# Performance work log

Measured on AMD Instinct MI355X. Metric: run time of the kernel, lower is better.

## Reference

```python
import jax, jax.numpy as jnp
import numpy as np

N, E, H = 20000, 320000, 5
IND, OUT = 64, 64
D2 = 2 * OUT          # 128
CAT = OUT + D2        # 192
BN_EPS = 1e-5


def _bn(x, g, b, m, v):
    # eval-mode BatchNorm1d
    return (x - m) * jax.lax.rsqrt(v + BN_EPS) * g + b


def _gcn(x, W, b, src, dst, n):
    # PyG GCNConv: add self-loops (already in src/dst), sym-normalized aggregation
    h = x @ W                                             # [N, C]
    deg = jax.ops.segment_sum(jnp.ones_like(dst, dtype=h.dtype), dst, num_segments=n)
    dinv = jnp.where(deg > 0, jax.lax.rsqrt(deg), 0.0)
    norm = dinv[src] * dinv[dst]                          # [E']
    out = jax.ops.segment_sum(h[src] * norm[:, None], dst, num_segments=n)
    return out + b


def _gat(x, W, att_src, att_dst, b, src, dst, n, heads, c):
    # PyG GATConv (concat=False): per-edge attention, segment softmax over dst
    hx = (x @ W).reshape(n, heads, c)                     # [N, H, C]
    a_s = jnp.einsum('nhc,hc->nh', hx, att_src)           # [N, H]
    a_d = jnp.einsum('nhc,hc->nh', hx, att_dst)
    e = jax.nn.leaky_relu(a_s[src] + a_d[dst], 0.2)       # [E', H]
    m = jax.ops.segment_max(e, dst, num_segments=n)       # every node has a self-loop
    w = jnp.exp(e - m[dst])
    den = jax.ops.segment_sum(w, dst, num_segments=n)
    alpha = w / den[dst]                                  # [E', H]
    out = jax.ops.segment_sum(hx[src] * alpha[:, :, None], dst, num_segments=n)  # [N,H,C]
    return out.mean(axis=1) + b


def setup_inputs() -> dict:
    key = jax.random.key(0)
    ks = iter(jax.random.split(key, 64))
    rn = lambda *s: jax.random.normal(next(ks), s, dtype=jnp.float32) * 0.05
    d = {}
    d['x_in'] = jax.random.normal(next(ks), (N, IND), dtype=jnp.float32)
    d['edge_index'] = jax.random.randint(next(ks), (2, E), 0, N, dtype=jnp.int64)
    # nn1: indim -> 2*indim -> outdim -> 2*outdim
    d['nn1_w1'], d['nn1_b1'] = rn(IND, 2 * IND), rn(2 * IND)
    d['nn1_w2'], d['nn1_b2'] = rn(2 * IND, OUT), rn(OUT)
    d['nn1_w3'], d['nn1_b3'] = rn(OUT, D2), rn(D2)
    # batchnorms (eval mode: gamma, beta, running mean/var)
    for name, dim in (('bn0', D2), ('bn1', D2), ('bn2', OUT)):
        d[name + '_g'] = rn(dim) + 1.0
        d[name + '_b'] = rn(dim)
        d[name + '_m'] = rn(dim)
        d[name + '_v'] = jax.random.uniform(next(ks), (dim,), jnp.float32, 0.5, 1.5)
    d['gcn1_w'], d['gcn1_b'] = rn(D2, D2), rn(D2)
    d['gat1_w'] = rn(D2, H * D2)
    d['gat1_as'], d['gat1_ad'], d['gat1_b'] = rn(H, D2), rn(H, D2), rn(D2)
    d['gcn2_w'], d['gcn2_b'] = rn(D2, OUT), rn(OUT)
    d['gat2_w'] = rn(OUT, H * OUT)
    d['gat2_as'], d['gat2_ad'], d['gat2_b'] = rn(H, OUT), rn(H, OUT), rn(OUT)
    # node_pred MLP: 192 -> 96 -> 48 -> 24 -> 1
    d['mlp_w1'], d['mlp_b1'] = rn(CAT, CAT // 2), rn(CAT // 2)
    d['mlp_w2'], d['mlp_b2'] = rn(CAT // 2, CAT // 4), rn(CAT // 4)
    d['mlp_w3'], d['mlp_b3'] = rn(CAT // 4, CAT // 8), rn(CAT // 8)
    d['mlp_w4'], d['mlp_b4'] = rn(CAT // 8, 1), rn(1)
    return d


def reference(x_in, edge_index,
              nn1_w1, nn1_b1, nn1_w2, nn1_b2, nn1_w3, nn1_b3,
              bn0_g, bn0_b, bn0_m, bn0_v,
              gcn1_w, gcn1_b, gat1_w, gat1_as, gat1_ad, gat1_b,
              gcn2_w, gcn2_b, gat2_w, gat2_as, gat2_ad, gat2_b,
              bn1_g, bn1_b, bn1_m, bn1_v,
              bn2_g, bn2_b, bn2_m, bn2_v,
              mlp_w1, mlp_b1, mlp_w2, mlp_b2, mlp_w3, mlp_b3, mlp_w4, mlp_b4):
    n = x_in.shape[0]
    loop = jnp.arange(n, dtype=edge_index.dtype)
    src = jnp.concatenate([edge_index[0], loop])   # self-loops (GCN & GAT defaults)
    dst = jnp.concatenate([edge_index[1], loop])

    sp = jax.nn.softplus
    x = sp(x_in @ nn1_w1 + nn1_b1)
    x = sp(x @ nn1_w2 + nn1_b2)
    x = x @ nn1_w3 + nn1_b3
    x = jax.nn.leaky_relu(_bn(x, bn0_g, bn0_b, bn0_m, bn0_v), 0.01)

    x1 = _gcn(x, gcn1_w, gcn1_b, src, dst, n)
    x1 = _gat(x1, gat1_w, gat1_as, gat1_ad, gat1_b, src, dst, n, H, D2)
    x1 = jax.nn.leaky_relu(_bn(x1, bn1_g, bn1_b, bn1_m, bn1_v), 0.01)
    skip1 = x + x1

    x2 = _gcn(skip1, gcn2_w, gcn2_b, src, dst, n)
    x2 = _gat(x2, gat2_w, gat2_as, gat2_ad, gat2_b, src, dst, n, H, OUT)
    x2 = jax.nn.leaky_relu(_bn(x2, bn2_g, bn2_b, bn2_m, bn2_v), 0.01)

    xf = jnp.concatenate([skip1, x2], axis=1)      # [N, 192]
    h = sp(xf @ mlp_w1 + mlp_b1)
    h = sp(h @ mlp_w2 + mlp_b2)
    h = sp(h @ mlp_w3 + mlp_b3)
    node_probs = jax.nn.sigmoid(h @ mlp_w4 + mlp_b4)   # [N, 1]
    return xf, node_probs
```

## Files before the change

kernel.cpp:

```cpp
#include <hip/hip_runtime.h>
#include <hip/hip_bf16.h>
#include <math.h>
#include <stdint.h>

typedef __hip_bfloat16 bf16;
typedef __hip_bfloat162 bf162;
typedef __attribute__((ext_vector_type(8))) short short8;
typedef __attribute__((ext_vector_type(4))) float f32x4;
#define HEADS 5

static inline long long cdivll(long long a, long long b){ return (a + b - 1) / b; }

__device__ __forceinline__ float b2f(bf16 v){ return __bfloat162float(v); }
__device__ __forceinline__ bf16 f2b(float v){ return __float2bfloat16(v); }
__device__ __forceinline__ short f2bs(float x){ bf16 b = __float2bfloat16(x); return *reinterpret_cast<short*>(&b); }
__device__ __forceinline__ float ldp(const void* p, long long i, int f32){
  return f32 ? ((const float*)p)[i] : b2f(((const bf16*)p)[i]);
}
__device__ __forceinline__ int eidx(const int* ei, long long i, int i64){
  return i64 ? ei[2 * i] : ei[i];
}
__device__ __forceinline__ float lrelu(float x, float a){ return x >= 0.f ? x : a * x; }
__device__ __forceinline__ float splus(float x){ return fmaxf(x, 0.f) + log1pf(expf(-fabsf(x))); }

__global__ void k_detect(const unsigned short* xh, const int* ei, int* flags){
  __shared__ int r0[256], r1[256];
  int t = threadIdx.x;
  int nan_cnt = 0;
  for (int i = t; i < 8192; i += 256){
    unsigned short u = xh[i];
    if (((u >> 7) & 0xFF) == 0xFF) nan_cnt++;
  }
  int odd_nz = 0;
  for (int i = 1 + 2 * t; i < 1024; i += 512) if (ei[i] != 0) odd_nz++;
  r0[t] = nan_cnt; r1[t] = odd_nz; __syncthreads();
  for (int o = 128; o > 0; o >>= 1){
    if (t < o){ r0[t] += r0[t + o]; r1[t] += r1[t + o]; }
    __syncthreads();
  }
  if (t == 0){
    flags[0] = (r0[0] > 0) ? 1 : 0;
    flags[1] = (r1[0] == 0) ? 1 : 0;
  }
}

__global__ void k_stampfill(bf16* out, long long n, float code){
  long long i = (long long)blockIdx.x * blockDim.x + threadIdx.x;
  if (i < n) out[i] = f2b(i == 0 ? code : 0.f);
}

__global__ void k_hist(const int* ei, int E, int N, int* counts, const int* flags){
  int i64 = flags[1];
  int e = blockIdx.x * blockDim.x + threadIdx.x;
  if (e >= E + N) return;
  int d = (e < E) ? eidx(ei, (long long)E + e, i64) : (e - E);
  atomicAdd(&counts[d], 1);
}
__global__ __launch_bounds__(1024) void k_scan(const int* counts, int* rowptr, int N){
  __shared__ int sums[1024];
  int t = threadIdx.x;
  int chunk = (N + 1023) / 1024;
  int start = t * chunk;
  int end = start + chunk; if (end > N) end = N;
  int s = 0;
  for (int i = start; i < end; ++i) s += counts[i];
  sums[t] = s; __syncthreads();
  for (int o = 1; o < 1024; o <<= 1){
    int v = (t >= o) ? sums[t - o] : 0;
    __syncthreads();
    sums[t] += v;
    __syncthreads();
  }
  int run = (t == 0) ? 0 : sums[t - 1];
  for (int i = start; i < end; ++i){ rowptr[i] = run; run += counts[i]; }
  if (t == 0) rowptr[N] = sums[1023];
}
__global__ void k_scatter(const int* ei, int E, int N, const int* rowptr, int* cursor,
                          unsigned short* colu, const int* flags){
  int i64 = flags[1];
  int e = blockIdx.x * blockDim.x + threadIdx.x;
  if (e >= E + N) return;
  int s, d;
  if (e < E){ s = eidx(ei, e, i64); d = eidx(ei, (long long)E + e, i64); }
  else { s = d = e - E; }
  int pos = rowptr[d] + atomicAdd(&cursor[d], 1);
  colu[pos] = (unsigned short)s;
}
__global__ void k_dinv(const int* rowptr, float* dinv, int N){
  int i = blockIdx.x * blockDim.x + threadIdx.x;
  if (i < N) dinv[i] = rsqrtf((float)(rowptr[i + 1] - rowptr[i]));
}

struct PackDesc { const void* W; int K, Kp, C, Cp, off, hk; };
struct PackArgs { PackDesc d[10]; int total; };
__global__ void k_packall(PackArgs P, bf16* WTA, int* cnt, int ncnt, const int* flags){
  int f32 = flags[0];
  int idx = blockIdx.x * blockDim.x + threadIdx.x;
  if (idx >= P.total){
    int z = idx - P.total;
    if (z < ncnt) cnt[z] = 0;
    return;
  }
  int base = 0;
#pragma unroll
  for (int s = 0; s < 10; ++s){
    int sz = P.d[s].Kp * P.d[s].Cp;
    if (idx < base + sz){
      int local = idx - base;
      int c = local / P.d[s].Kp;
      int k = local - c * P.d[s].Kp;
      float v;
      if (P.d[s].hk){
        int h = k / P.d[s].K;
        int kk = k - h * P.d[s].K;
        v = (c < P.d[s].C)
          ? ldp(P.d[s].W, (long long)kk * (P.d[s].hk * P.d[s].C) + h * P.d[s].C + c, f32) : 0.f;
      } else {
        v = (k < P.d[s].K && c < P.d[s].C)
          ? ldp(P.d[s].W, (long long)k * P.d[s].C + c, f32) : 0.f;
      }
      WTA[P.d[s].off + local] = f2b(v);
      return;
    }
    base += sz;
  }
}

__global__ void k_att_fold(const void* w1, const void* as1, const void* ad1,
                           const void* w2, const void* as2, const void* ad2,
                           bf16* wta, const int* flags){
  int f32 = flags[0];
  int idx = blockIdx.x * blockDim.x + threadIdx.x;
  if (idx < 8192){
    int c = idx >> 7, k = idx & 127;
    float v = 0.f;
    if (c < 10){
      int h = (c < 5) ? c : c - 5;
      const void* aw = (c < 5) ? as1 : ad1;
      for (int j = 0; j < 128; ++j)
        v = fmaf(ldp(w1, (long long)k * 640 + h * 128 + j, f32), ldp(aw, h * 128 + j, f32), v);
    }
    wta[186368 + idx] = f2b(v);
  } else if (idx < 12288){
    int l = idx - 8192;
    int c = l >> 6, k = l & 63;
    float v = 0.f;
    if (c < 10){
      int h = (c < 5) ? c : c - 5;
      const void* aw = (c < 5) ? as2 : ad2;
      for (int j = 0; j < 64; ++j)
        v = fmaf(ldp(w2, (long long)k * 320 + h * 64 + j, f32), ldp(aw, h * 64 + j, f32), v);
    }
    wta[194560 + l] = f2b(v);
  }
}

__global__ __launch_bounds__(256) void k_proj128(
    const void* in, int ik, int ldin, const bf16* WT, bf16* outb,
    int N, int Cp, const int* flags)
{
  __shared__ float red[2][16][68];
  int f32 = flags[0];
  int use_b16 = (ik == 2 && !f32);
  int t = threadIdx.x;
  int wave = t >> 6, lane = t & 63;
  int quad = lane >> 4, l15 = lane & 15;
  int rowgrp = wave & 1, kh = wave >> 1;
  int mbase = blockIdx.x * 32 + rowgrp * 16;
  int c0 = blockIdx.y * 64;
  f32x4 acc[4];
#pragma unroll
  for (int j = 0; j < 4; ++j) acc[j] = (f32x4){0.f, 0.f, 0.f, 0.f};

  int m = mbase + l15; if (m > N - 1) m = N - 1;

#pragma unroll
  for (int ki = 0; ki < 2; ++ki){
    int ka = kh * 64 + ki * 32 + quad * 8;
    short8 af;
    if (use_b16){
      af = *(const short8*)((const bf16*)in + (size_t)m * ldin + ka);
    } else {
      const float* p = (const float*)in + (size_t)m * ldin + ka;
      float4 v0 = *(const float4*)p;
      float4 v1 = *(const float4*)(p + 4);
      af[0] = f2bs(v0.x); af[1] = f2bs(v0.y); af[2] = f2bs(v0.z); af[3] = f2bs(v0.w);
      af[4] = f2bs(v1.x); af[5] = f2bs(v1.y); af[6] = f2bs(v1.z); af[7] = f2bs(v1.w);
    }
#pragma unroll
    for (int j = 0; j < 4; ++j){
      short8 bvv = *(const short8*)(WT + (size_t)(c0 + 16 * j + l15) * 128 + ka);
      acc[j] = __builtin_amdgcn_mfma_f32_16x16x32_bf16(af, bvv, acc[j], 0, 0, 0);
    }
  }

  if (kh == 1){
#pragma unroll
    for (int j = 0; j < 4; ++j)
#pragma unroll
      for (int r = 0; r < 4; ++r)
        red[rowgrp][quad * 4 + r][16 * j + l15] = acc[j][r];
  }
  __syncthreads();
  if (kh == 1) return;
#pragma unroll
  for (int j = 0; j < 4; ++j)
#pragma unroll
    for (int r = 0; r < 4; ++r)
      acc[j][r] += red[rowgrp][quad * 4 + r][16 * j + l15];

#pragma unroll
  for (int j = 0; j < 4; ++j){
    int c = c0 + 16 * j + l15;
#pragma unroll
    for (int r = 0; r < 4; ++r){
      int n = mbase + quad * 4 + r;
      if (n < N) outb[(size_t)n * Cp + c] = f2b(acc[j][r]);
    }
  }
}

__global__ __launch_bounds__(256) void k_nn1f(
    const void* xin, const bf16* WTA,
    const void* b1, const void* b2, const void* b3,
    const void* g0, const void* bb0, const void* m0, const void* v0,
    float* X, int N, const int* flags)
{
  __shared__ bf16 s1[4][16][136];
  __shared__ bf16 s2[4][16][72];
  int f32 = flags[0];
  int t = threadIdx.x, wave = t >> 6, lane = t & 63;
  int quad = lane >> 4, l15 = lane & 15;
  int mbase = blockIdx.x * 64 + wave * 16;
  int m = mbase + l15; if (m > N - 1) m = N - 1;

  f32x4 a1[8];
#pragma unroll
  for (int j = 0; j < 8; ++j) a1[j] = (f32x4){0.f, 0.f, 0.f, 0.f};
#pragma unroll
  for (int k0 = 0; k0 < 64; k0 += 32){
    int ka = k0 + quad * 8;
    short8 af;
    if (!f32){
      af = *(const short8*)((const bf16*)xin + (size_t)m * 64 + ka);
    } else {
      const float* p = (const float*)xin + (size_t)m * 64 + ka;
      float4 v0 = *(const float4*)p;
      float4 v1 = *(const float4*)(p + 4);
      af[0] = f2bs(v0.x); af[1] = f2bs(v0.y); af[2] = f2bs(v0.z); af[3] = f2bs(v0.w);
      af[4] = f2bs(v1.x); af[5] = f2bs(v1.y); af[6] = f2bs(v1.z); af[7] = f2bs(v1.w);
    }
#pragma unroll
    for (int j = 0; j < 8; ++j){
      short8 bvv = *(const short8*)(WTA + (size_t)(16 * j + l15) * 64 + ka);
      a1[j] = __builtin_amdgcn_mfma_f32_16x16x32_bf16(af, bvv, a1[j], 0, 0, 0);
    }
  }
#pragma unroll
  for (int j = 0; j < 8; ++j){
    int c = 16 * j + l15;
    float bi = ldp(b1, c, f32);
#pragma unroll
    for (int r = 0; r < 4; ++r)
      s1[wave][quad * 4 + r][c] = f2b(splus(a1[j][r] + bi));
  }
  __syncthreads();

  f32x4 a2[4];
#pragma unroll
  for (int j = 0; j < 4; ++j) a2[j] = (f32x4){0.f, 0.f, 0.f, 0.f};
#pragma unroll
  for (int k0 = 0; k0 < 128; k0 += 32){
    int ka = k0 + quad * 8;
    short8 af = *(const short8*)&s1[wave][l15][ka];
#pragma unroll
    for (int j = 0; j < 4; ++j){
      short8 bvv = *(const short8*)(WTA + 8192 + (size_t)(16 * j + l15) * 128 + ka);
      a2[j] = __builtin_amdgcn_mfma_f32_16x16x32_bf16(af, bvv, a2[j], 0, 0, 0);
    }
  }
#pragma unroll
  for (int j = 0; j < 4; ++j){
    int c = 16 * j + l15;
    float bi = ldp(b2, c, f32);
#pragma unroll
    for (int r = 0; r < 4; ++r)
      s2[wave][quad * 4 + r][c] = f2b(splus(a2[j][r] + bi));
  }
  __syncthreads();

  f32x4 a3[8];
#pragma unroll
  for (int j = 0; j < 8; ++j) a3[j] = (f32x4){0.f, 0.f, 0.f, 0.f};
#pragma unroll
  for (int k0 = 0; k0 < 64; k0 += 32){
    int ka = k0 + quad * 8;
    short8 af = *(const short8*)&s2[wave][l15][ka];
#pragma unroll
    for (int j = 0; j < 8; ++j){
      short8 bvv = *(const short8*)(WTA + 16384 + (size_t)(16 * j + l15) * 64 + ka);
      a3[j] = __builtin_amdgcn_mfma_f32_16x16x32_bf16(af, bvv, a3[j], 0, 0, 0);
    }
  }
#pragma unroll
  for (int j = 0; j < 8; ++j){
    int c = 16 * j + l15;
    float bi = ldp(b3, c, f32);
    float g = ldp(g0, c, f32), be = ldp(bb0, c, f32), mm = ldp(m0, c, f32);
    float iv = rsqrtf(ldp(v0, c, f32) + 1e-5f);
#pragma unroll
    for (int r = 0; r < 4; ++r){
      int n = mbase + quad * 4 + r;
      if (n >= N) continue;
      float y = a3[j][r] + bi;
      y = (y - mm) * iv * g + be;
      X[(size_t)n * 128 + c] = lrelu(y, 0.01f);
    }
  }
}

__global__ __launch_bounds__(256) void k_mlpf(
    const void* dout, const bf16* WTA,
    const void* b1, const void* b2, const void* b3,
    const void* w4, const void* b4, void* outfin, int N, const int* flags)
{
  __shared__ bf16 s1[4][16][104];
  __shared__ bf16 s2[4][16][72];
  int f32 = flags[0];
  int t = threadIdx.x, wave = t >> 6, lane = t & 63;
  int quad = lane >> 4, l15 = lane & 15;
  int mbase = blockIdx.x * 64 + wave * 16;
  int m = mbase + l15; if (m > N - 1) m = N - 1;

  f32x4 a1[6];
#pragma unroll
  for (int j = 0; j < 6; ++j) a1[j] = (f32x4){0.f, 0.f, 0.f, 0.f};
#pragma unroll
  for (int k0 = 0; k0 < 192; k0 += 32){
    int ka = k0 + quad * 8;
    short8 af;
    if (!f32){
      af = *(const short8*)((const bf16*)dout + (size_t)m * 192 + ka);
    } else {
      const float* p = (const float*)dout + (size_t)m * 192 + ka;
      float4 v0 = *(const float4*)p;
      float4 v1 = *(const float4*)(p + 4);
      af[0] = f2bs(v0.x); af[1] = f2bs(v0.y); af[2] = f2bs(v0.z); af[3] = f2bs(v0.w);
      af[4] = f2bs(v1.x); af[5] = f2bs(v1.y); af[6] = f2bs(v1.z); af[7] = f2bs(v1.w);
    }
#pragma unroll
    for (int j = 0; j < 6; ++j){
      short8 bvv = *(const short8*)(WTA + 151552 + (size_t)(16 * j + l15) * 192 + ka);
      a1[j] = __builtin_amdgcn_mfma_f32_16x16x32_bf16(af, bvv, a1[j], 0, 0, 0);
    }
  }
#pragma unroll
  for (int j = 0; j < 6; ++j){
    int c = 16 * j + l15;
    float bi = ldp(b1, c, f32);
#pragma unroll
    for (int r = 0; r < 4; ++r)
      s1[wave][quad * 4 + r][c] = f2b(splus(a1[j][r] + bi));
  }
  __syncthreads();

  f32x4 a2[3];
#pragma unroll
  for (int j = 0; j < 3; ++j) a2[j] = (f32x4){0.f, 0.f, 0.f, 0.f};
#pragma unroll
  for (int k0 = 0; k0 < 96; k0 += 32){
    int ka = k0 + quad * 8;
    short8 af = *(const short8*)&s1[wave][l15][ka];
#pragma unroll
    for (int j = 0; j < 3; ++j){
      short8 bvv = *(const short8*)(WTA + 176128 + (size_t)(16 * j + l15) * 96 + ka);
      a2[j] = __builtin_amdgcn_mfma_f32_16x16x32_bf16(af, bvv, a2[j], 0, 0, 0);
    }
  }
#pragma unroll
  for (int j = 0; j < 4; ++j){
    int c = 16 * j + l15;
    if (j < 3){
      float bi = ldp(b2, c, f32);
#pragma unroll
      for (int r = 0; r < 4; ++r)
        s2[wave][quad * 4 + r][c] = f2b(splus(a2[j][r] + bi));
    } else {
#pragma unroll
      for (int r = 0; r < 4; ++r)
        s2[wave][quad * 4 + r][c] = f2b(0.f);
    }
  }
  __syncthreads();

  f32x4 a3[2];
#pragma unroll
  for (int j = 0; j < 2; ++j) a3[j] = (f32x4){0.f, 0.f, 0.f, 0.f};
#pragma unroll
  for (int k0 = 0; k0 < 64; k0 += 32){
    int ka = k0 + quad * 8;
    short8 af = *(const short8*)&s2[wave][l15][ka];
#pragma unroll
    for (int j = 0; j < 2; ++j){
      short8 bvv = *(const short8*)(WTA + 182272 + (size_t)(16 * j + l15) * 64 + ka);
      a3[j] = __builtin_amdgcn_mfma_f32_16x16x32_bf16(af, bvv, a3[j], 0, 0, 0);
    }
  }
  float pr[4] = {0.f, 0.f, 0.f, 0.f};
#pragma unroll
  for (int j = 0; j < 2; ++j){
    int c = 16 * j + l15;
    float w = (c < 24) ? ldp(w4, c, f32) : 0.f;
    float bi = (c < 24) ? ldp(b3, c, f32) : 0.f;
#pragma unroll
    for (int r = 0; r < 4; ++r)
      pr[r] = fmaf(splus(a3[j][r] + bi), w, pr[r]);
  }
#pragma unroll
  for (int r = 0; r < 4; ++r){
#pragma unroll
    for (int o = 1; o < 16; o <<= 1) pr[r] += __shfl_xor(pr[r], o);
    int n = mbase + quad * 4 + r;
    if (l15 == 0 && n < N){
      float p = 1.f / (1.f + expf(-(pr[r] + ldp(b4, 0, f32))));
      long long oi = (long long)N * 192 + n;
      if (f32) ((float*)outfin)[oi] = p; else ((bf16*)outfin)[oi] = f2b(p);
    }
  }
}

__global__ __launch_bounds__(256) void k_gcn_csr(
    const int* rowptr, const unsigned short* colu, const bf16* h,
    const float* dinv, const void* bias, bf16* outb, int N, int C,
    const bf16* watt, float* asd, const int* flags)
{
  int f32 = flags[0];
  int wid = (blockIdx.x * 256 + threadIdx.x) >> 6;
  int lane = threadIdx.x & 63;
  if (wid >= N) return;
  int i0 = rowptr[wid], i1 = rowptr[wid + 1];
  float dr = dinv[wid];
  if (C == 128){
    int coff = lane << 1;
    float ax[4] = {0.f, 0.f, 0.f, 0.f}, ay[4] = {0.f, 0.f, 0.f, 0.f};
    int i = i0;
    for (; i + 3 < i1; i += 4){
      int s[4] = {colu[i], colu[i + 1], colu[i + 2], colu[i + 3]};
#pragma unroll
      for (int e = 0; e < 4; ++e){
        bf162 v = *(const bf162*)(h + (size_t)s[e] * 128 + coff);
        float f = dinv[s[e]];
        ax[e] = fmaf(f, b2f(v.x), ax[e]); ay[e] = fmaf(f, b2f(v.y), ay[e]);
      }
    }
    for (; i < i1; ++i){
      int s0 = colu[i];
      bf162 v = *(const bf162*)(h + (size_t)s0 * 128 + coff);
      float f = dinv[s0];
      ax[0] = fmaf(f, b2f(v.x), ax[0]); ay[0] = fmaf(f, b2f(v.y), ay[0]);
    }
    float sx = (ax[0] + ax[1]) + (ax[2] + ax[3]);
    float sy = (ay[0] + ay[1]) + (ay[2] + ay[3]);
    float vx = sx * dr + ldp(bias, coff, f32);
    float vy = sy * dr + ldp(bias, coff + 1, f32);
    bf162 o; o.x = f2b(vx); o.y = f2b(vy);
    *(bf162*)(outb + (size_t)wid * 128 + coff) = o;
    if (watt){
      float myv = 0.f;
#pragma unroll
      for (int hh = 0; hh < 10; ++hh){
        bf162 w = *(const bf162*)(watt + hh * 128 + coff);
        float p = vx * b2f(w.x) + vy * b2f(w.y);
#pragma unroll
        for (int o2 = 1; o2 < 64; o2 <<= 1) p += __shfl_xor(p, o2);
        if (lane == hh) myv = p;
      }
      if (lane < 10) asd[(size_t)wid * 10 + lane] = myv;
    }
  } else {
    int half = lane >> 5, hl = lane & 31;
    int coff = hl << 1;
    float ax = 0.f, ay = 0.f, bx = 0.f, by = 0.f;
    int i = i0;
    for (; i + 3 < i1; i += 4){
      int sA = colu[i + half], sB = colu[i + 2 + half];
      bf162 vA = *(const bf162*)(h + (size_t)sA * 64 + coff);
      bf162 vB = *(const bf162*)(h + (size_t)sB * 64 + coff);
      float fA = dinv[sA], fB = dinv[sB];
      ax = fmaf(fA, b2f(vA.x), ax); ay = fmaf(fA, b2f(vA.y), ay);
      bx = fmaf(fB, b2f(vB.x), bx); by = fmaf(fB, b2f(vB.y), by);
    }
    for (; i + 1 < i1; i += 2){
      int s = colu[i + half];
      bf162 v = *(const bf162*)(h + (size_t)s * 64 + coff);
      float f = dinv[s];
      ax = fmaf(f, b2f(v.x), ax); ay = fmaf(f, b2f(v.y), ay);
    }
    if (i < i1 && half == 0){
      int s = colu[i];
      bf162 v = *(const bf162*)(h + (size_t)s * 64 + coff);
      float f = dinv[s];
      ax = fmaf(f, b2f(v.x), ax); ay = fmaf(f, b2f(v.y), ay);
    }
    ax += bx; ay += by;
    ax += __shfl_xor(ax, 32);
    ay += __shfl_xor(ay, 32);
    float vx = ax * dr + ldp(bias, coff, f32);
    float vy = ay * dr + ldp(bias, coff + 1, f32);
    if (half == 0){
      bf162 o; o.x = f2b(vx); o.y = f2b(vy);
      *(bf162*)(outb + (size_t)wid * 64 + coff) = o;
    }
    if (watt){
      float myv = 0.f;
#pragma unroll
      for (int hh = 0; hh < 10; ++hh){
        bf162 w = *(const bf162*)(watt + hh * 64 + coff);
        float p = vx * b2f(w.x) + vy * b2f(w.y);
#pragma unroll
        for (int o2 = 1; o2 < 32; o2 <<= 1) p += __shfl_xor(p, o2);
        if (lane == hh) myv = p;
      }
      if (lane < 10) asd[(size_t)wid * 10 + lane] = myv;
    }
  }
}

template<int K>
__global__ __launch_bounds__(1024) void k_gat_proj(
    const int* rowptr, const unsigned short* colu, const bf16* bbx,
    const float* asd, const bf16* WT, const void* bias,
    const void* bg, const void* bbp, const void* bm, const void* bv,
    const float* skip, void* dout, int c2off, int N, const int* flags)
{
  constexpr int KP  = HEADS * K;
  constexpr int AGP = (K == 128) ? 648 : 328;
  constexpr int C   = K;
  constexpr int NCG = C / 16;
  constexpr int KSEG = KP / 2;
  __shared__ bf16 agg[16][AGP];
  __shared__ float als[16][HEADS][64];
  __shared__ unsigned short ssrc[16][64];
  int f32 = flags[0];
  int t = threadIdx.x, wave = t >> 6, lane = t & 63;
  int quad = lane >> 4, l15 = lane & 15;
  int rb = blockIdx.x * 16;

  int wid = rb + wave;
  if (wid < N){
    int i0 = rowptr[wid], i1 = rowptr[wid + 1];
    float adr[HEADS];
#pragma unroll
    for (int h = 0; h < HEADS; ++h) adr[h] = asd[(size_t)wid * 10 + 5 + h];
    float mx[HEADS];
#pragma unroll
    for (int h = 0; h < HEADS; ++h) mx[h] = -1e30f;
    for (int i = i0 + lane; i < i1; i += 64){
      int s = colu[i];
#pragma unroll
      for (int h = 0; h < HEADS; ++h){
        float e = lrelu(asd[(size_t)s * 10 + h] + adr[h], 0.2f);
        mx[h] = fmaxf(mx[h], e);
      }
    }
#pragma unroll
    for (int h = 0; h < HEADS; ++h)
      for (int o = 32; o > 0; o >>= 1) mx[h] = fmaxf(mx[h], __shfl_xor(mx[h], o));
    float den[HEADS];
#pragma unroll
    for (int h = 0; h < HEADS; ++h) den[h] = 0.f;
    for (int i = i0 + lane; i < i1; i += 64){
      int s = colu[i];
#pragma unroll
      for (int h = 0; h < HEADS; ++h){
        float e = lrelu(asd[(size_t)s * 10 + h] + adr[h], 0.2f);
        den[h] += expf(e - mx[h]);
      }
    }
#pragma unroll
    for (int h = 0; h < HEADS; ++h){
      for (int o = 32; o > 0; o >>= 1) den[h] += __shfl_xor(den[h], o);
      den[h] = 1.f / (den[h] * (float)HEADS);
    }
    if constexpr (K == 128){
      int coff = lane << 1;
      float ax[HEADS], ay[HEADS];
#pragma unroll
      for (int h = 0; h < HEADS; ++h){ ax[h] = 0.f; ay[h] = 0.f; }
      for (int base = i0; base < i1; base += 64){
        int iend = i1 - base; if (iend > 64) iend = 64;
        int i = base + lane;
        if (i < i1){
          int s = colu[i];
          ssrc[wave][lane] = (unsigned short)s;
#pragma unroll
          for (int h = 0; h < HEADS; ++h){
            float e = lrelu(asd[(size_t)s * 10 + h] + adr[h], 0.2f);
            als[wave][h][lane] = expf(e - mx[h]) * den[h];
          }
        }
        asm volatile("s_waitcnt lgkmcnt(0)" ::: "memory");
        int j = 0;
        for (; j + 3 < iend; j += 4){
          int s4[4];
#pragma unroll
          for (int e = 0; e < 4; ++e) s4[e] = ssrc[wave][j + e];
          bf162 v[4];
#pragma unroll
          for (int e = 0; e < 4; ++e) v[e] = *(const bf162*)(bbx + (size_t)s4[e] * 128 + coff);
#pragma unroll
          for (int e = 0; e < 4; ++e){
            float fx = b2f(v[e].x), fy = b2f(v[e].y);
#pragma unroll
            for (int h = 0; h < HEADS; ++h){
              float a = als[wave][h][j + e];
              ax[h] = fmaf(a, fx, ax[h]); ay[h] = fmaf(a, fy, ay[h]);
            }
          }
        }
        for (; j < iend; ++j){
          int s = ssrc[wave][j];
          bf162 v = *(const bf162*)(bbx + (size_t)s * 128 + coff);
          float fx = b2f(v.x), fy = b2f(v.y);
#pragma unroll
          for (int h = 0; h < HEADS; ++h){
            float a = als[wave][h][j];
            ax[h] = fmaf(a, fx, ax[h]); ay[h] = fmaf(a, fy, ay[h]);
          }
        }
      }
#pragma unroll
      for (int h = 0; h < HEADS; ++h){
        bf162 o; o.x = f2b(ax[h]); o.y = f2b(ay[h]);
        *(bf162*)&agg[wave][h * 128 + coff] = o;
      }
    } else {
      int half = lane >> 5, hl = lane & 31;
      int coff = hl << 1;
      float ax[HEADS], ay[HEADS];
#pragma unroll
      for (int h = 0; h < HEADS; ++h){ ax[h] = 0.f; ay[h] = 0.f; }
      for (int base = i0; base < i1; base += 64){
        int iend = i1 - base; if (iend > 64) iend = 64;
        int i = base + lane;
        if (i < i1){
          int s = colu[i];
          ssrc[wave][lane] = (unsigned short)s;
#pragma unroll
          for (int h = 0; h < HEADS; ++h){
            float e = lrelu(asd[(size_t)s * 10 + h] + adr[h], 0.2f);
            als[wave][h][lane] = expf(e - mx[h]) * den[h];
          }
        }
        asm volatile("s_waitcnt lgkmcnt(0)" ::: "memory");
        int j = 0;
        for (; j + 3 < iend; j += 4){
          int sA = ssrc[wave][j + half], sB = ssrc[wave][j + 2 + half];
          bf162 vA = *(const bf162*)(bbx + (size_t)sA * 64 + coff);
          bf162 vB = *(const bf162*)(bbx + (size_t)sB * 64 + coff);
          float Ax = b2f(vA.x), Ay = b2f(vA.y), Bx = b2f(vB.x), By = b2f(vB.y);
#pragma unroll
          for (int h = 0; h < HEADS; ++h){
            float aA = als[wave][h][j + half], aB = als[wave][h][j + 2 + half];
            ax[h] = fmaf(aA, Ax, ax[h]); ay[h] = fmaf(aA, Ay, ay[h]);
            ax[h] = fmaf(aB, Bx, ax[h]); ay[h] = fmaf(aB, By, ay[h]);
          }
        }
        for (; j + 1 < iend; j += 2){
          int s = ssrc[wave][j + half];
          bf162 v = *(const bf162*)(bbx + (size_t)s * 64 + coff);
          float fx = b2f(v.x), fy = b2f(v.y);
#pragma unroll
          for (int h = 0; h < HEADS; ++h){
            float a = als[wave][h][j + half];
            ax[h] = fmaf(a, fx, ax[h]); ay[h] = fmaf(a, fy, ay[h]);
          }
        }
        if (j < iend && half == 0){
          int s = ssrc[wave][j];
          bf162 v = *(const bf162*)(bbx + (size_t)s * 64 + coff);
          float fx = b2f(v.x), fy = b2f(v.y);
#pragma unroll
          for (int h = 0; h < HEADS; ++h){
            float a = als[wave][h][j];
            ax[h] = fmaf(a, fx, ax[h]); ay[h] = fmaf(a, fy, ay[h]);
          }
        }
      }
#pragma unroll
      for (int h = 0; h < HEADS; ++h){
        ax[h] += __shfl_xor(ax[h], 32);
        ay[h] += __shfl_xor(ay[h], 32);
      }
      if (half == 0){
#pragma unroll
        for (int h = 0; h < HEADS; ++h){
          bf162 o; o.x = f2b(ax[h]); o.y = f2b(ay[h]);
          *(bf162*)&agg[wave][h * 64 + coff] = o;
        }
      }
    }
  }
  __syncthreads();

  auto red = reinterpret_cast<float(*)[16][17]>(&als[0][0][0]);
  int cg = wave & (NCG - 1);
  int kh = wave / NCG;
  f32x4 acc = (f32x4){0.f, 0.f, 0.f, 0.f};
  if (kh < 2){
#pragma unroll
    for (int ks = 0; ks < KSEG; ks += 32){
      int ka = kh * KSEG + ks + quad * 8;
      short8 af = *(const short8*)&agg[l15][ka];
      short8 bvv = *(const short8*)(WT + (size_t)(cg * 16 + l15) * KP + ka);
      acc = __builtin_amdgcn_mfma_f32_16x16x32_bf16(af, bvv, acc, 0, 0, 0);
    }
  }
  if (kh == 1){
#pragma unroll
    for (int r = 0; r < 4; ++r)
      red[cg][quad * 4 + r][l15] = acc[r];
  }
  __syncthreads();
  if (kh != 0) return;
#pragma unroll
  for (int r = 0; r < 4; ++r)
    acc[r] += red[cg][quad * 4 + r][l15];

  int c = cg * 16 + l15;
  float bi = ldp(bias, c, f32);
  float g = ldp(bg, c, f32), be = ldp(bbp, c, f32), mm = ldp(bm, c, f32);
  float iv = rsqrtf(ldp(bv, c, f32) + 1e-5f);
#pragma unroll
  for (int r = 0; r < 4; ++r){
    int n = rb + quad * 4 + r;
    if (n >= N) continue;
    float y = acc[r] + bi;
    y = (y - mm) * iv * g + be;
    y = lrelu(y, 0.01f);
    if (skip) y += skip[(size_t)n * 128 + c];
    size_t o = (size_t)n * 192 + c2off + c;
    if (f32) ((float*)dout)[o] = y; else ((bf16*)dout)[o] = f2b(y);
  }
}

extern "C" void kernel_launch(void* const* d_in, const int* in_sizes, int n_in,
                              void* d_out, int out_size, void* d_ws, size_t ws_size,
                              hipStream_t stream)
{
  const void* x_in   = d_in[0];
  const int*  ei     = (const int*)d_in[1];
  const void *nn1_w1 = d_in[2], *nn1_b1 = d_in[3], *nn1_w2 = d_in[4], *nn1_b2 = d_in[5];
  const void *nn1_w3 = d_in[6], *nn1_b3 = d_in[7];
  const void *bn0_g = d_in[8],  *bn0_b = d_in[9],  *bn0_m = d_in[10], *bn0_v = d_in[11];
  const void *bn1_g = d_in[12], *bn1_b = d_in[13], *bn1_m = d_in[14], *bn1_v = d_in[15];
  const void *bn2_g = d_in[16], *bn2_b = d_in[17], *bn2_m = d_in[18], *bn2_v = d_in[19];
  const void *gcn1_w = d_in[20], *gcn1_b = d_in[21];
  const void *gat1_w = d_in[22], *gat1_as = d_in[23], *gat1_ad = d_in[24], *gat1_b = d_in[25];
  const void *gcn2_w = d_in[26], *gcn2_b = d_in[27];
  const void *gat2_w = d_in[28], *gat2_as = d_in[29], *gat2_ad = d_in[30], *gat2_b = d_in[31];
  const void *mlp_w1 = d_in[32], *mlp_b1 = d_in[33], *mlp_w2 = d_in[34], *mlp_b2 = d_in[35];
  const void *mlp_w3 = d_in[36], *mlp_b3 = d_in[37], *mlp_w4 = d_in[38], *mlp_b4 = d_in[39];
  (void)n_in;

  const int N  = in_sizes[0] / 64;
  const int E  = in_sizes[1] / 2;
  const int Ep = E + N;
  const int TB = 256;

  if ((long long)out_size != (long long)N * 193 || N > 65535){
    k_stampfill<<<(int)cdivll(out_size, TB), TB, 0, stream>>>((bf16*)d_out, out_size, 8192.f);
    return;
  }
  size_t need = 2900ull * (size_t)N + 500000ull;
  if (ws_size < need){
    k_stampfill<<<(int)cdivll(out_size, TB), TB, 0, stream>>>((bf16*)d_out, out_size, 1024.f);
    return;
  }

  char* wsb = (char*)d_ws;
  int*   FLAGS = (int*)wsb;
  float* X    = (float*)(wsb + 16);
  float* A    = X + (size_t)N * 128;
  float* B    = A + (size_t)N * 128;
  float* DINV = B + (size_t)N * 128;
  float* AS   = DINV + N;
  int*   ROWP = (int*)(AS + (size_t)N * 2 * HEADS);
  unsigned short* COLU = (unsigned short*)(ROWP + N + 1);
  bf16*  HX   = (bf16*)(COLU + ((Ep + 7) & ~7));
  bf16*  WTA  = (bf16*)(((uintptr_t)(HX + (size_t)N * 640) + 15) & ~(uintptr_t)15);
  bf16*  BB   = (bf16*)A;
  int* CNT = (int*)AS;
  int* CUR = CNT + N;
  const int ATT1_OFF = 186368;
  const int ATT2_OFF = 194560;

  k_detect<<<1, 256, 0, stream>>>((const unsigned short*)x_in, ei, FLAGS);

  PackArgs P;
  P.d[0] = {nn1_w1,  64, 64, 128, 128, 0, 0};
  P.d[1] = {nn1_w2, 128,128,  64,  64, 8192, 0};
  P.d[2] = {nn1_w3,  64, 64, 128, 128, 16384, 0};
  P.d[3] = {gcn1_w, 128,128, 128, 128, 24576, 0};
  P.d[4] = {gat1_w, 128,640, 128, 128, 40960, 5};
  P.d[5] = {gcn2_w, 128,128,  64,  64, 122880, 0};
  P.d[6] = {gat2_w,  64,320,  64,  64, 131072, 5};
  P.d[7] = {mlp_w1, 192,192,  96, 128, 151552, 0};
  P.d[8] = {mlp_w2,  96, 96,  48,  64, 176128, 0};
  P.d[9] = {mlp_w3,  48, 64,  24,  64, 182272, 0};
  P.total = 186368;
  k_packall<<<(int)cdivll(P.total + 2 * N, TB), TB, 0, stream>>>(P, WTA, CNT, 2 * N, FLAGS);
  k_att_fold<<<48, 256, 0, stream>>>(gat1_w, gat1_as, gat1_ad, gat2_w, gat2_as, gat2_ad, WTA, FLAGS);

  k_hist<<<(int)cdivll(Ep, TB), TB, 0, stream>>>(ei, E, N, CNT, FLAGS);
  k_scan<<<1, 1024, 0, stream>>>(CNT, ROWP, N);
  k_scatter<<<(int)cdivll(Ep, TB), TB, 0, stream>>>(ei, E, N, ROWP, CUR, COLU, FLAGS);
  k_dinv<<<(int)cdivll(N, TB), TB, 0, stream>>>(ROWP, DINV, N);

  int rowsg = (int)cdivll(N, 4);
  int rowsf = (int)cdivll(N, 64);
  int rows16 = (int)cdivll(N, 16);

  k_nn1f<<<rowsf, 256, 0, stream>>>(x_in, WTA, nn1_b1, nn1_b2, nn1_b3,
                                    bn0_g, bn0_b, bn0_m, bn0_v, X, N, FLAGS);

  k_proj128<<<dim3((unsigned)cdivll(N, 32), 2), 256, 0, stream>>>(
      X, 0, 128, WTA + 24576, HX, N, 128, FLAGS);
  k_gcn_csr<<<rowsg, 256, 0, stream>>>(ROWP, COLU, HX, DINV, gcn1_b, BB, N, 128,
                                       WTA + ATT1_OFF, AS, FLAGS);

  k_gat_proj<128><<<rows16, 1024, 0, stream>>>(ROWP, COLU, BB, AS, WTA + 40960, gat1_b,
      bn1_g, bn1_b, bn1_m, bn1_v, X, d_out, 0, N, FLAGS);

  k_proj128<<<dim3((unsigned)cdivll(N, 32), 1), 256, 0, stream>>>(
      d_out, 2, 192, WTA + 122880, HX, N, 64, FLAGS);
  k_gcn_csr<<<rowsg, 256, 0, stream>>>(ROWP, COLU, HX, DINV, gcn2_b, BB, N, 64,
                                       WTA + ATT2_OFF, AS, FLAGS);

  k_gat_proj<64><<<rows16, 1024, 0, stream>>>(ROWP, COLU, BB, AS, WTA + 131072, gat2_b,
      bn2_g, bn2_b, bn2_m, bn2_v, nullptr, d_out, 128, N, FLAGS);

  k_mlpf<<<rowsf, 256, 0, stream>>>(d_out, WTA, mlp_b1, mlp_b2, mlp_b3,
                                    mlp_w4, mlp_b4, d_out, N, FLAGS);
}
```

Baseline: 461.6 us.

## Fuse GCN weight projections into nn1 and GAT1 epilogues, drop proj kernels

Removes the two standalone k_proj128 launches. The GCN1 projection now runs in k_nn1f from the bf16 activations staged in shared memory, and the GCN2 projection runs at the end of k_gat_proj<128> from the freshly computed skip output held in shared memory. This avoids re-reading X and d_out from global memory and saves two launches. In exchange the fused kernels need extra MFMA work, more registers and extra barriers, which may cut occupancy.

```diff
diff --git a/kernel.cpp b/kernel.cpp
--- a/kernel.cpp
+++ b/kernel.cpp
@@ -155,76 +155,11 @@
   }
 }
 
-__global__ __launch_bounds__(256) void k_proj128(
-    const void* in, int ik, int ldin, const bf16* WT, bf16* outb,
-    int N, int Cp, const int* flags)
-{
-  __shared__ float red[2][16][68];
-  int f32 = flags[0];
-  int use_b16 = (ik == 2 && !f32);
-  int t = threadIdx.x;
-  int wave = t >> 6, lane = t & 63;
-  int quad = lane >> 4, l15 = lane & 15;
-  int rowgrp = wave & 1, kh = wave >> 1;
-  int mbase = blockIdx.x * 32 + rowgrp * 16;
-  int c0 = blockIdx.y * 64;
-  f32x4 acc[4];
-#pragma unroll
-  for (int j = 0; j < 4; ++j) acc[j] = (f32x4){0.f, 0.f, 0.f, 0.f};
-
-  int m = mbase + l15; if (m > N - 1) m = N - 1;
-
-#pragma unroll
-  for (int ki = 0; ki < 2; ++ki){
-    int ka = kh * 64 + ki * 32 + quad * 8;
-    short8 af;
-    if (use_b16){
-      af = *(const short8*)((const bf16*)in + (size_t)m * ldin + ka);
-    } else {
-      const float* p = (const float*)in + (size_t)m * ldin + ka;
-      float4 v0 = *(const float4*)p;
-      float4 v1 = *(const float4*)(p + 4);
-      af[0] = f2bs(v0.x); af[1] = f2bs(v0.y); af[2] = f2bs(v0.z); af[3] = f2bs(v0.w);
-      af[4] = f2bs(v1.x); af[5] = f2bs(v1.y); af[6] = f2bs(v1.z); af[7] = f2bs(v1.w);
-    }
-#pragma unroll
-    for (int j = 0; j < 4; ++j){
-      short8 bvv = *(const short8*)(WT + (size_t)(c0 + 16 * j + l15) * 128 + ka);
-      acc[j] = __builtin_amdgcn_mfma_f32_16x16x32_bf16(af, bvv, acc[j], 0, 0, 0);
-    }
-  }
-
-  if (kh == 1){
-#pragma unroll
-    for (int j = 0; j < 4; ++j)
-#pragma unroll
-      for (int r = 0; r < 4; ++r)
-        red[rowgrp][quad * 4 + r][16 * j + l15] = acc[j][r];
-  }
-  __syncthreads();
-  if (kh == 1) return;
-#pragma unroll
-  for (int j = 0; j < 4; ++j)
-#pragma unroll
-    for (int r = 0; r < 4; ++r)
-      acc[j][r] += red[rowgrp][quad * 4 + r][16 * j + l15];
-
-#pragma unroll
-  for (int j = 0; j < 4; ++j){
-    int c = c0 + 16 * j + l15;
-#pragma unroll
-    for (int r = 0; r < 4; ++r){
-      int n = mbase + quad * 4 + r;
-      if (n < N) outb[(size_t)n * Cp + c] = f2b(acc[j][r]);
-    }
-  }
-}
-
 __global__ __launch_bounds__(256) void k_nn1f(
     const void* xin, const bf16* WTA,
     const void* b1, const void* b2, const void* b3,
     const void* g0, const void* bb0, const void* m0, const void* v0,
-    float* X, int N, const int* flags)
+    float* X, bf16* hx, int N, const int* flags)
 {
   __shared__ bf16 s1[4][16][136];
   __shared__ bf16 s2[4][16][72];
@@ -245,10 +180,10 @@
       af = *(const short8*)((const bf16*)xin + (size_t)m * 64 + ka);
     } else {
       const float* p = (const float*)xin + (size_t)m * 64 + ka;
-      float4 v0 = *(const float4*)p;
-      float4 v1 = *(const float4*)(p + 4);
-      af[0] = f2bs(v0.x); af[1] = f2bs(v0.y); af[2] = f2bs(v0.z); af[3] = f2bs(v0.w);
-      af[4] = f2bs(v1.x); af[5] = f2bs(v1.y); af[6] = f2bs(v1.z); af[7] = f2bs(v1.w);
+      float4 v0v = *(const float4*)p;
+      float4 v1v = *(const float4*)(p + 4);
+      af[0] = f2bs(v0v.x); af[1] = f2bs(v0v.y); af[2] = f2bs(v0v.z); af[3] = f2bs(v0v.w);
+      af[4] = f2bs(v1v.x); af[5] = f2bs(v1v.y); af[6] = f2bs(v1v.z); af[7] = f2bs(v1v.w);
     }
 #pragma unroll
     for (int j = 0; j < 8; ++j){
@@ -314,7 +249,33 @@
       if (n >= N) continue;
       float y = a3[j][r] + bi;
       y = (y - mm) * iv * g + be;
-      X[(size_t)n * 128 + c] = lrelu(y, 0.01f);
+      y = lrelu(y, 0.01f);
+      X[(size_t)n * 128 + c] = y;
+      s1[wave][quad * 4 + r][c] = f2b(y);
+    }
+  }
+  __syncthreads();
+
+  f32x4 a4[8];
+#pragma unroll
+  for (int j = 0; j < 8; ++j) a4[j] = (f32x4){0.f, 0.f, 0.f, 0.f};
+#pragma unroll
+  for (int k0 = 0; k0 < 128; k0 += 32){
+    int ka = k0 + quad * 8;
+    short8 af = *(const short8*)&s1[wave][l15][ka];
+#pragma unroll
+    for (int j = 0; j < 8; ++j){
+      short8 bvv = *(const short8*)(WTA + 24576 + (size_t)(16 * j + l15) * 128 + ka);
+      a4[j] = __builtin_amdgcn_mfma_f32_16x16x32_bf16(af, bvv, a4[j], 0, 0, 0);
+    }
+  }
+#pragma unroll
+  for (int j = 0; j < 8; ++j){
+    int c = 16 * j + l15;
+#pragma unroll
+    for (int r = 0; r < 4; ++r){
+      int n = mbase + quad * 4 + r;
+      if (n < N) hx[(size_t)n * 128 + c] = f2b(a4[j][r]);
     }
   }
 }
@@ -531,7 +492,8 @@
     const int* rowptr, const unsigned short* colu, const bf16* bbx,
     const float* asd, const bf16* WT, const void* bias,
     const void* bg, const void* bbp, const void* bm, const void* bv,
-    const float* skip, void* dout, int c2off, int N, const int* flags)
+    const float* skip, void* dout, int c2off,
+    const bf16* WT2, bf16* hx, int N, const int* flags)
 {
   constexpr int KP  = HEADS * K;
   constexpr int AGP = (K == 128) ? 648 : 328;
@@ -703,7 +665,7 @@
   }
   __syncthreads();
 
-  auto red = reinterpret_cast<float(*)[16][17]>(&als[0][0][0]);
+  auto red = reinterpret_cast<float(*)[16][20]>(&als[0][0][0]);
   int cg = wave & (NCG - 1);
   int kh = wave / NCG;
   f32x4 acc = (f32x4){0.f, 0.f, 0.f, 0.f};
@@ -722,25 +684,59 @@
       red[cg][quad * 4 + r][l15] = acc[r];
   }
   __syncthreads();
-  if (kh != 0) return;
-#pragma unroll
-  for (int r = 0; r < 4; ++r)
-    acc[r] += red[cg][quad * 4 + r][l15];
-
-  int c = cg * 16 + l15;
-  float bi = ldp(bias, c, f32);
-  float g = ldp(bg, c, f32), be = ldp(bbp, c, f32), mm = ldp(bm, c, f32);
-  float iv = rsqrtf(ldp(bv, c, f32) + 1e-5f);
-#pragma unroll
-  for (int r = 0; r < 4; ++r){
-    int n = rb + quad * 4 + r;
-    if (n >= N) continue;
-    float y = acc[r] + bi;
-    y = (y - mm) * iv * g + be;
-    y = lrelu(y, 0.01f);
-    if (skip) y += skip[(size_t)n * 128 + c];
-    size_t o = (size_t)n * 192 + c2off + c;
-    if (f32) ((float*)dout)[o] = y; else ((bf16*)dout)[o] = f2b(y);
+  if (kh == 0){
+#pragma unroll
+    for (int r = 0; r < 4; ++r)
+      acc[r] += red[cg][quad * 4 + r][l15];
+    int c = cg * 16 + l15;
+    float bi = ldp(bias, c, f32);
+    float g = ldp(bg, c, f32), be = ldp(bbp, c, f32), mm = ldp(bm, c, f32);
+    float iv = rsqrtf(ldp(bv, c, f32) + 1e-5f);
+#pragma unroll
+    for (int r = 0; r < 4; ++r){
+      int n = rb + quad * 4 + r;
+      if (n >= N) continue;
+      float y = acc[r] + bi;
+      y = (y - mm) * iv * g + be;
+      y = lrelu(y, 0.01f);
+      if (skip) y += skip[(size_t)n * 128 + c];
+      size_t o = (size_t)n * 192 + c2off + c;
+      if (f32) ((float*)dout)[o] = y; else ((bf16*)dout)[o] = f2b(y);
+      if (WT2) agg[quad * 4 + r][c] = f2b(y);
+    }
+  }
+
+  if constexpr (K == 128){
+    if (WT2){
+      __syncthreads();
+      int cg2 = wave & 3, kh2 = wave >> 2;
+      f32x4 a2 = (f32x4){0.f, 0.f, 0.f, 0.f};
+      int ka = kh2 * 32 + quad * 8;
+      short8 af = *(const short8*)&agg[l15][ka];
+      short8 bvv = *(const short8*)(WT2 + (size_t)(cg2 * 16 + l15) * 128 + ka);
+      a2 = __builtin_amdgcn_mfma_f32_16x16x32_bf16(af, bvv, a2, 0, 0, 0);
+      auto red2 = reinterpret_cast<float(*)[16][20]>(&als[0][0][0]);
+      if (kh2 > 0){
+        int slot = (kh2 - 1) * 4 + cg2;
+#pragma unroll
+        for (int r = 0; r < 4; ++r)
+          red2[slot][quad * 4 + r][l15] = a2[r];
+      }
+      __syncthreads();
+      if (kh2 == 0){
+#pragma unroll
+        for (int s = 0; s < 3; ++s)
+#pragma unroll
+          for (int r = 0; r < 4; ++r)
+            a2[r] += red2[s * 4 + cg2][quad * 4 + r][l15];
+        int c2 = cg2 * 16 + l15;
+#pragma unroll
+        for (int r = 0; r < 4; ++r){
+          int n = rb + quad * 4 + r;
+          if (n < N) hx[(size_t)n * 64 + c2] = f2b(a2[r]);
+        }
+      }
+    }
   }
 }
 
@@ -822,23 +818,19 @@
   int rows16 = (int)cdivll(N, 16);
 
   k_nn1f<<<rowsf, 256, 0, stream>>>(x_in, WTA, nn1_b1, nn1_b2, nn1_b3,
-                                    bn0_g, bn0_b, bn0_m, bn0_v, X, N, FLAGS);
-
-  k_proj128<<<dim3((unsigned)cdivll(N, 32), 2), 256, 0, stream>>>(
-      X, 0, 128, WTA + 24576, HX, N, 128, FLAGS);
+                                    bn0_g, bn0_b, bn0_m, bn0_v, X, HX, N, FLAGS);
+
   k_gcn_csr<<<rowsg, 256, 0, stream>>>(ROWP, COLU, HX, DINV, gcn1_b, BB, N, 128,
                                        WTA + ATT1_OFF, AS, FLAGS);
 
   k_gat_proj<128><<<rows16, 1024, 0, stream>>>(ROWP, COLU, BB, AS, WTA + 40960, gat1_b,
-      bn1_g, bn1_b, bn1_m, bn1_v, X, d_out, 0, N, FLAGS);
-
-  k_proj128<<<dim3((unsigned)cdivll(N, 32), 1), 256, 0, stream>>>(
-      d_out, 2, 192, WTA + 122880, HX, N, 64, FLAGS);
+      bn1_g, bn1_b, bn1_m, bn1_v, X, d_out, 0, WTA + 122880, HX, N, FLAGS);
+
   k_gcn_csr<<<rowsg, 256, 0, stream>>>(ROWP, COLU, HX, DINV, gcn2_b, BB, N, 64,
                                        WTA + ATT2_OFF, AS, FLAGS);
 
   k_gat_proj<64><<<rows16, 1024, 0, stream>>>(ROWP, COLU, BB, AS, WTA + 131072, gat2_b,
-      bn2_g, bn2_b, bn2_m, bn2_v, nullptr, d_out, 128, N, FLAGS);
+      bn2_g, bn2_b, bn2_m, bn2_v, nullptr, d_out, 128, nullptr, nullptr, N, FLAGS);
 
   k_mlpf<<<rowsf, 256, 0, stream>>>(d_out, WTA, mlp_b1, mlp_b2, mlp_b3,
                                     mlp_w4, mlp_b4, d_out, N, FLAGS);
```

Result: no change. 455.7 us (-1.3%).
